# Optimization experiments

Measured on AMD Instinct MI355X. Metric: run time of the kernel, lower is better.

Reference implementation:

```python
import jax, jax.numpy as jnp
import numpy as np

B, S, D, H = 4, 2048, 1024, 16
HD = D // H
SCALE = float(np.sqrt(HD))

def setup_inputs() -> dict:
    key = jax.random.key(0)
    ks = jax.random.split(key, 6)
    std = 1.0 / np.sqrt(D)
    return {
        "x": jax.random.normal(ks[0], (B, S, D), dtype=jnp.float32),
        "Wq": jax.random.normal(ks[1], (D, D), dtype=jnp.float32) * std,
        "Wk": jax.random.normal(ks[2], (D, D), dtype=jnp.float32) * std,
        "Wv": jax.random.normal(ks[3], (D, D), dtype=jnp.float32) * std,
        "Wo": jax.random.normal(ks[4], (D, D), dtype=jnp.float32) * std,
        "bo": jnp.zeros((D,), dtype=jnp.float32),
    }

def reference(x, Wq, Wk, Wv, Wo, bo):
    b, s, _ = x.shape
    # nn.Linear(y) = y @ W.T ; project then split heads -> [B,H,S,HD]
    def proj(W):
        return (x @ W.T).reshape(b, s, H, HD).transpose(0, 2, 1, 3)
    q, k, v = proj(Wq), proj(Wk), proj(Wv)
    scores = jnp.einsum("bhqd,bhkd->bhqk", q, k) / SCALE
    causal = jnp.triu(jnp.ones((s, s), dtype=bool), k=1)
    scores = jnp.where(causal[None, None, :, :], -jnp.inf, scores)
    attn = jax.nn.softmax(scores, axis=-1)  # dropout is identity in eval mode
    out = jnp.einsum("bhqk,bhkd->bhqd", attn, v)
    out = out.transpose(0, 2, 1, 3).reshape(b, s, D)
    return out @ Wo.T + bo
```

## Files before the change

kernel.cpp:

```cpp
#include <hip/hip_runtime.h>
#include <hip/hip_bf16.h>

constexpr int Sc = 2048, Dc = 1024;

typedef __attribute__((ext_vector_type(8))) short bf16x8;
typedef __attribute__((ext_vector_type(4))) short short4v;
typedef __attribute__((ext_vector_type(4))) float f32x4;
typedef __attribute__((ext_vector_type(16))) float f32x16;

static __device__ __forceinline__ short f2bf(float f) {
  __hip_bfloat16 h = __float2bfloat16(f);
  short s; __builtin_memcpy(&s, &h, 2);
  return s;
}

static __device__ __forceinline__ unsigned int cvtpk(float lo, float hi) {
  unsigned int r;
  asm("v_cvt_pk_bf16_f32 %0, %1, %2" : "=v"(r) : "v"(lo), "v"(hi));
  return r;
}

typedef __attribute__((address_space(3))) short lds_short_t;

static __device__ __forceinline__ void gload16(const short* g, lds_short_t* l) {
  __builtin_amdgcn_global_load_lds(
      (const __attribute__((address_space(1))) unsigned int*)g,
      (__attribute__((address_space(3))) unsigned int*)l, 16, 0, 0);
}

__global__ __launch_bounds__(256) void cvt_f32_bf16(const float* __restrict__ src,
                                                    short* __restrict__ dst,
                                                    int n4) {
  int i = blockIdx.x * 256 + threadIdx.x;
  if (i >= n4) return;
  float4 v = ((const float4*)src)[i];
  short4v o;
  o.x = f2bf(v.x); o.y = f2bf(v.y); o.z = f2bf(v.z); o.w = f2bf(v.w);
  ((short4v*)dst)[i] = o;
}

__global__ __launch_bounds__(256) void cvt_w4(const float* __restrict__ w0,
                                              const float* __restrict__ w1,
                                              const float* __restrict__ w2,
                                              const float* __restrict__ w3,
                                              short* __restrict__ dst) {
  const int y = blockIdx.y;
  const float* src = (y == 0) ? w0 : (y == 1) ? w1 : (y == 2) ? w2 : w3;
  int i = blockIdx.x * 256 + threadIdx.x;
  float4 v = ((const float4*)src)[i];
  short4v o;
  o.x = f2bf(v.x); o.y = f2bf(v.y); o.z = f2bf(v.z); o.w = f2bf(v.w);
  ((short4v*)(dst))[(size_t)y * 262144 + i] = o;
}

template <int MODE>
__global__ __launch_bounds__(256) void gemm_mfma(
    const short* __restrict__ A, const short* __restrict__ W,
    const float* __restrict__ bias, short* __restrict__ Qb,
    short* __restrict__ Kb, short* __restrict__ Vt, float* __restrict__ outF) {
  __shared__ short As[128 * 32];
  __shared__ short Bs[128 * 32];
  const int tid = threadIdx.x;
  const int m0 = blockIdx.x * 128, n0 = blockIdx.y * 128;
  const int lane = tid & 63, w = tid >> 6;
  const int wr = w >> 1, wc = w & 1;
  const int ll = lane & 15, lh = lane >> 4;

  lds_short_t* As3 = (lds_short_t*)As;
  lds_short_t* Bs3 = (lds_short_t*)Bs;

  const short* Abase[2];
  const short* Wbase[2];
#pragma unroll
  for (int i = 0; i < 2; ++i) {
    int slot = i * 256 + w * 64 + lane;
    int row = slot >> 2;
    int col = ((slot & 3) ^ (row & 3)) * 8;
    Abase[i] = A + (size_t)(m0 + row) * 1024 + col;
    Wbase[i] = W + (size_t)(n0 + row) * 1024 + col;
  }

  f32x4 acc[4][4] = {};

  for (int k0 = 0; k0 < 1024; k0 += 32) {
    __syncthreads();
#pragma unroll
    for (int i = 0; i < 2; ++i) {
      gload16(Abase[i] + k0, As3 + (i * 256 + w * 64) * 8);
      gload16(Wbase[i] + k0, Bs3 + (i * 256 + w * 64) * 8);
    }
    __syncthreads();

    bf16x8 fa[4], fb[4];
#pragma unroll
    for (int mi = 0; mi < 4; ++mi) {
      int r = wr * 64 + mi * 16 + ll;
      fa[mi] = *(const bf16x8*)&As[r * 32 + ((lh ^ (ll & 3)) * 8)];
    }
#pragma unroll
    for (int ni = 0; ni < 4; ++ni) {
      int r = wc * 64 + ni * 16 + ll;
      fb[ni] = *(const bf16x8*)&Bs[r * 32 + ((lh ^ (ll & 3)) * 8)];
    }
#pragma unroll
    for (int mi = 0; mi < 4; ++mi)
#pragma unroll
      for (int ni = 0; ni < 4; ++ni)
        acc[mi][ni] = __builtin_amdgcn_mfma_f32_16x16x32_bf16(
            fa[mi], fb[ni], acc[mi][ni], 0, 0, 0);
  }

#pragma unroll
  for (int mi = 0; mi < 4; ++mi) {
#pragma unroll
    for (int ni = 0; ni < 4; ++ni) {
#pragma unroll
      for (int r = 0; r < 4; ++r) {
        int row = m0 + wr * 64 + mi * 16 + lh * 4 + r;
        int n = n0 + wc * 64 + ni * 16 + ll;
        float v = acc[mi][ni][r];
        if constexpr (MODE == 1) {
          outF[(size_t)row * 1024 + n] = v + bias[n];
        } else {
          if (n < 1024) {
            Qb[(size_t)row * 1024 + n] = f2bf(v * 0.18033688f);
          } else if (n < 2048) {
            Kb[(size_t)row * 1024 + (n - 1024)] = f2bf(v);
          } else {
            int c = n - 2048, hh = c >> 6, dd = c & 63;
            int bb = row >> 11, ss = row & 2047;
            Vt[(size_t)((bb * 16 + hh) * 64 + dd) * 2048 + ss] = f2bf(v);
          }
        }
      }
    }
  }
}

__global__ __launch_bounds__(256, 3) void attn_v7(const short* __restrict__ Q,
                                                  const short* __restrict__ K,
                                                  const short* __restrict__ Vt,
                                                  short* __restrict__ AO) {
  __shared__ short Ks[2][64 * 64];
  __shared__ short Vs[2][64 * 64];
  const int tid = threadIdx.x, lane = tid & 63, w = tid >> 6;
  const int l31 = lane & 31, lh2 = lane >> 5;
  const int id = blockIdx.x;
  const int bh = id & 63;
  const int qs = id >> 6;
  const int jj = qs >> 2;
  const int qb = (jj == 0) ? qs : (jj == 1) ? 19 - qs : (jj == 2) ? qs - 4 : 23 - qs;
  const int b = bh >> 4, h = bh & 15;
  const int q0 = qb * 128;
  const int R = q0 + w * 32;
  const int kw_last = (R + 31) >> 6;
  const int kb_max = (q0 + 127) >> 6;
  const short* Qp = Q + (size_t)b * Sc * Dc + h * 64;
  const short* Kp = K + (size_t)b * Sc * Dc + h * 64;
  const short* Vp = Vt + (size_t)bh * 64 * Sc;

  lds_short_t* Ks3 = (lds_short_t*)Ks;
  lds_short_t* Vs3 = (lds_short_t*)Vs;

  bf16x8 qf[4];
#pragma unroll
  for (int dk = 0; dk < 4; ++dk)
    qf[dk] = *(const bf16x8*)&Qp[(size_t)(R + l31) * Dc + dk * 16 + lh2 * 8];

  const short* Kst[2];
  const short* Vst[2];
  int ldsOff[2];
#pragma unroll
  for (int i = 0; i < 2; ++i) {
    int slot = i * 256 + w * 64 + lane;
    int row = slot >> 3;
    int col = ((slot & 7) ^ (row & 7)) * 8;
    Kst[i] = Kp + (size_t)row * 1024 + col;
    Vst[i] = Vp + (size_t)row * 2048 + col;
    ldsOff[i] = (i * 256 + w * 64) * 8;
  }

  f32x16 o0 = {}, o1 = {};
  float lrun = 0.f;

#pragma unroll
  for (int i = 0; i < 2; ++i) {
    gload16(Kst[i], Ks3 + ldsOff[i]);
    gload16(Vst[i], Vs3 + ldsOff[i]);
  }
  int cur = 0;

  for (int kb = 0; kb <= kb_max; ++kb) {
    __syncthreads();
    if (kb < kb_max) {
      int nb = cur ^ 1;
#pragma unroll
      for (int i = 0; i < 2; ++i) {
        gload16(Kst[i] + (size_t)(kb + 1) * 65536, Ks3 + nb * 4096 + ldsOff[i]);
        gload16(Vst[i] + (kb + 1) * 64, Vs3 + nb * 4096 + ldsOff[i]);
      }
    }

    if (kb <= kw_last) {
      const bool diag = (kb == kw_last);
      const bool skipHi = diag && ((R & 63) == 0);

      f32x16 sv0 = {}, sv1 = {};
      {
        const int row = l31, rx = row & 7;
#pragma unroll
        for (int dk = 0; dk < 4; ++dk) {
          bf16x8 kf =
              *(const bf16x8*)&Ks[cur][row * 64 + (((dk * 2 + lh2) ^ rx) * 8)];
          sv0 = __builtin_amdgcn_mfma_f32_32x32x16_bf16(kf, qf[dk], sv0, 0, 0, 0);
        }
      }
      if (!skipHi) {
        const int row = 32 + l31, rx = row & 7;
#pragma unroll
        for (int dk = 0; dk < 4; ++dk) {
          bf16x8 kf =
              *(const bf16x8*)&Ks[cur][row * 64 + (((dk * 2 + lh2) ^ rx) * 8)];
          sv1 = __builtin_amdgcn_mfma_f32_32x32x16_bf16(kf, qf[dk], sv1, 0, 0, 0);
        }
      }

      float ts = 0.f;
      if (!diag) {
#pragma unroll
        for (int r = 0; r < 16; ++r) {
          float e0 = exp2f(sv0[r]);
          float e1 = exp2f(sv1[r]);
          sv0[r] = e0; sv1[r] = e1;
          ts += e0 + e1;
        }
      } else if (skipHi) {
#pragma unroll
        for (int r = 0; r < 16; ++r) {
          int kl = (r & 3) + 8 * (r >> 2) + 4 * lh2;
          float e = (kl > l31) ? 0.f : exp2f(sv0[r]);
          sv0[r] = e;
          ts += e;
        }
      } else {
#pragma unroll
        for (int r = 0; r < 16; ++r) {
          float e = exp2f(sv0[r]);
          sv0[r] = e;
          ts += e;
        }
#pragma unroll
        for (int r = 0; r < 16; ++r) {
          int kl = (r & 3) + 8 * (r >> 2) + 4 * lh2;
          float e = (kl > l31) ? 0.f : exp2f(sv1[r]);
          sv1[r] = e;
          ts += e;
        }
      }
      lrun += ts;

      short4v pa[8];
#pragma unroll
      for (int t = 0; t < 4; ++t) {
        union { unsigned int u[2]; short4v s; } pk;
        pk.u[0] = cvtpk(sv0[4 * t + 0], sv0[4 * t + 1]);
        pk.u[1] = cvtpk(sv0[4 * t + 2], sv0[4 * t + 3]);
        pa[t] = pk.s;
      }
      if (skipHi) {
        const int r0 = l31, rx0 = r0 & 7;
        const int r1 = 32 + l31, rx1 = r1 & 7;
#pragma unroll
        for (int t = 0; t < 4; ++t) {
          short4v vb0 =
              *(const short4v*)&Vs[cur][r0 * 64 + ((t ^ rx0) * 8) + lh2 * 4];
          o0 = __builtin_amdgcn_mfma_f32_32x32x8bf16_1k(pa[t], vb0, o0, 0, 0, 0);
          short4v vb1 =
              *(const short4v*)&Vs[cur][r1 * 64 + ((t ^ rx1) * 8) + lh2 * 4];
          o1 = __builtin_amdgcn_mfma_f32_32x32x8bf16_1k(pa[t], vb1, o1, 0, 0, 0);
        }
      } else {
#pragma unroll
        for (int t = 0; t < 4; ++t) {
          union { unsigned int u[2]; short4v s; } pk;
          pk.u[0] = cvtpk(sv1[4 * t + 0], sv1[4 * t + 1]);
          pk.u[1] = cvtpk(sv1[4 * t + 2], sv1[4 * t + 3]);
          pa[4 + t] = pk.s;
        }
        const int r0 = l31, rx0 = r0 & 7;
        const int r1 = 32 + l31, rx1 = r1 & 7;
#pragma unroll
        for (int t = 0; t < 8; ++t) {
          short4v vb0 =
              *(const short4v*)&Vs[cur][r0 * 64 + ((t ^ rx0) * 8) + lh2 * 4];
          o0 = __builtin_amdgcn_mfma_f32_32x32x8bf16_1k(pa[t], vb0, o0, 0, 0, 0);
        }
#pragma unroll
        for (int t = 0; t < 8; ++t) {
          short4v vb1 =
              *(const short4v*)&Vs[cur][r1 * 64 + ((t ^ rx1) * 8) + lh2 * 4];
          o1 = __builtin_amdgcn_mfma_f32_32x32x8bf16_1k(pa[t], vb1, o1, 0, 0, 0);
        }
      }
    }
    cur ^= 1;
  }

  float ltot = lrun + __shfl_xor(lrun, 32);
#pragma unroll
  for (int r = 0; r < 16; ++r) {
    int qr = (r & 3) + 8 * (r >> 2) + 4 * lh2;
    float lq = __shfl(ltot, qr);
    float inv = 1.0f / lq;
    int rowg = R + qr;
    AO[((size_t)(b * Sc + rowg)) * Dc + h * 64 + l31] = f2bf(o0[r] * inv);
    AO[((size_t)(b * Sc + rowg)) * Dc + h * 64 + 32 + l31] = f2bf(o1[r] * inv);
  }
}

extern "C" void kernel_launch(void* const* d_in, const int* in_sizes, int n_in,
                              void* d_out, int out_size, void* d_ws,
                              size_t ws_size, hipStream_t stream) {
  const float* x = (const float*)d_in[0];
  const float* Wq = (const float*)d_in[1];
  const float* Wk = (const float*)d_in[2];
  const float* Wv = (const float*)d_in[3];
  const float* Wo = (const float*)d_in[4];
  const float* bo = (const float*)d_in[5];
  float* out = (float*)d_out;

  short* Qb = (short*)d_out;
  short* Kb = Qb + (size_t)8192 * 1024;
  short* xb = (short*)d_ws;
  short* AOb = xb;
  short* Wc = xb + (size_t)8192 * 1024;
  short* Vt = Wc + (size_t)4096 * 1024;

  dim3 blk(256);
  hipLaunchKernelGGL(cvt_f32_bf16, dim3(8192), blk, 0, stream, x, xb, 2097152);
  hipLaunchKernelGGL(cvt_w4, dim3(1024, 4), blk, 0, stream, Wq, Wk, Wv, Wo, Wc);

  hipLaunchKernelGGL((gemm_mfma<0>), dim3(64, 24), blk, 0, stream, xb, Wc,
                     (const float*)nullptr, Qb, Kb, Vt, (float*)nullptr);

  hipLaunchKernelGGL(attn_v7, dim3(1024), blk, 0, stream, Qb, Kb, Vt, AOb);

  hipLaunchKernelGGL((gemm_mfma<1>), dim3(64, 8), blk, 0, stream, AOb,
                     Wc + (size_t)3072 * 1024, bo, (short*)nullptr,
                     (short*)nullptr, (short*)nullptr, out);
}
```

Measured before the change: 193.3 us.

## Replace QKV projection GEMM with 256x256-tile 8-wave ping-pong kernel

Splits the templated GEMM into a dedicated QKV projection kernel and a separate output-projection kernel. The QKV kernel uses 512 threads and 256x256 output tiles with 64-wide K steps, split into four 128x128 quadrants. Each quadrant's global load into a double-buffered LDS area is interleaved with the MFMA work of another, and s_setprio is raised around the MFMA bursts. It also adds an XCD-aware block remap. The aim is more reuse per loaded tile and better load/compute overlap in the largest GEMM, at the cost of higher register use and 128KB of LDS, which limits occupancy.

```diff
diff --git a/kernel.cpp b/kernel.cpp
--- a/kernel.cpp
+++ b/kernel.cpp
@@ -53,11 +53,197 @@
   ((short4v*)(dst))[(size_t)y * 262144 + i] = o;
 }
 
-template <int MODE>
-__global__ __launch_bounds__(256) void gemm_mfma(
+__global__ __launch_bounds__(512, 2) void gemm_qkv_8p(
     const short* __restrict__ A, const short* __restrict__ W,
-    const float* __restrict__ bias, short* __restrict__ Qb,
-    short* __restrict__ Kb, short* __restrict__ Vt, float* __restrict__ outF) {
+    short* __restrict__ Qb, short* __restrict__ Kb, short* __restrict__ Vt) {
+  __shared__ short lds[2][4][8192];
+  const int tid = threadIdx.x, lane = tid & 63, w = tid >> 6;
+  const int wm = w >> 2, wn = w & 3;
+  const int ll = lane & 15, lh = lane >> 4;
+  const int wg = ((int)blockIdx.x & 7) * 48 + ((int)blockIdx.x >> 3);
+  const int m0 = (wg / 12) * 256, n0 = (wg % 12) * 256;
+
+  lds_short_t* L3 = (lds_short_t*)&lds[0][0][0];
+
+  const short* Asrc[2];
+  const short* Bsrc[2];
+  int dstOff[2];
+#pragma unroll
+  for (int i = 0; i < 2; ++i) {
+    int slot = i * 512 + tid;
+    int ridx = slot >> 3, g = slot & 7;
+    int gp = g ^ (ridx & 7);
+    Asrc[i] = A + (size_t)(m0 + (ridx & 63) + ((ridx >> 6) << 7)) * 1024 + gp * 8;
+    Bsrc[i] = W + (size_t)(n0 + ((ridx >> 5) << 6) + (ridx & 31)) * 1024 + gp * 8;
+    dstOff[i] = (i * 512 + w * 64) * 8;
+  }
+
+  f32x4 acc[8][4] = {};
+  bf16x8 fa[4][2];
+  bf16x8 fb0[2][2];
+  bf16x8 fb1[2][2];
+
+#pragma unroll
+  for (int i = 0; i < 2; ++i) gload16(Asrc[i], L3 + 0 * 8192 + dstOff[i]);
+#pragma unroll
+  for (int i = 0; i < 2; ++i) gload16(Bsrc[i], L3 + 1 * 8192 + dstOff[i]);
+#pragma unroll
+  for (int i = 0; i < 2; ++i)
+    gload16(Bsrc[i] + 32 * 1024, L3 + 2 * 8192 + dstOff[i]);
+#pragma unroll
+  for (int i = 0; i < 2; ++i)
+    gload16(Asrc[i] + 64 * 1024, L3 + 3 * 8192 + dstOff[i]);
+  asm volatile("s_waitcnt vmcnt(4)" ::: "memory");
+  __builtin_amdgcn_s_barrier();
+
+  for (int kt = 0; kt < 16; ++kt) {
+    const int c = kt & 1;
+    const int cb = c * 32768, nb = (c ^ 1) * 32768;
+    const int kn = (kt + 1) * 64;
+
+#pragma unroll
+    for (int mi = 0; mi < 4; ++mi) {
+      int ridx = wm * 64 + mi * 16 + ll;
+#pragma unroll
+      for (int kh = 0; kh < 2; ++kh)
+        fa[mi][kh] = *(const bf16x8*)&lds[c][0][ridx * 64 +
+                                               (((kh * 4 + lh) ^ (ll & 7)) * 8)];
+    }
+#pragma unroll
+    for (int ni = 0; ni < 2; ++ni) {
+      int ridx = wn * 32 + ni * 16 + ll;
+#pragma unroll
+      for (int kh = 0; kh < 2; ++kh)
+        fb0[ni][kh] = *(const bf16x8*)&lds[c][1][ridx * 64 +
+                                                 (((kh * 4 + lh) ^ (ll & 7)) * 8)];
+    }
+    if (kt < 15) {
+#pragma unroll
+      for (int i = 0; i < 2; ++i)
+        gload16(Asrc[i] + kn, L3 + nb + 0 * 8192 + dstOff[i]);
+    }
+    asm volatile("s_waitcnt vmcnt(4)" ::: "memory");
+    __builtin_amdgcn_s_barrier();
+    __builtin_amdgcn_s_setprio(1);
+#pragma unroll
+    for (int mi = 0; mi < 4; ++mi)
+#pragma unroll
+      for (int ni = 0; ni < 2; ++ni)
+#pragma unroll
+        for (int kh = 0; kh < 2; ++kh)
+          acc[mi][ni] = __builtin_amdgcn_mfma_f32_16x16x32_bf16(
+              fa[mi][kh], fb0[ni][kh], acc[mi][ni], 0, 0, 0);
+    __builtin_amdgcn_s_setprio(0);
+    __builtin_amdgcn_s_barrier();
+
+#pragma unroll
+    for (int ni = 0; ni < 2; ++ni) {
+      int ridx = wn * 32 + ni * 16 + ll;
+#pragma unroll
+      for (int kh = 0; kh < 2; ++kh)
+        fb1[ni][kh] = *(const bf16x8*)&lds[c][2][ridx * 64 +
+                                                 (((kh * 4 + lh) ^ (ll & 7)) * 8)];
+    }
+    if (kt < 15) {
+#pragma unroll
+      for (int i = 0; i < 2; ++i)
+        gload16(Bsrc[i] + kn, L3 + nb + 1 * 8192 + dstOff[i]);
+    }
+    asm volatile("s_waitcnt vmcnt(4)" ::: "memory");
+    __builtin_amdgcn_s_barrier();
+    __builtin_amdgcn_s_setprio(1);
+#pragma unroll
+    for (int mi = 0; mi < 4; ++mi)
+#pragma unroll
+      for (int ni = 0; ni < 2; ++ni)
+#pragma unroll
+        for (int kh = 0; kh < 2; ++kh)
+          acc[mi][2 + ni] = __builtin_amdgcn_mfma_f32_16x16x32_bf16(
+              fa[mi][kh], fb1[ni][kh], acc[mi][2 + ni], 0, 0, 0);
+    __builtin_amdgcn_s_setprio(0);
+    __builtin_amdgcn_s_barrier();
+
+#pragma unroll
+    for (int mi = 0; mi < 4; ++mi) {
+      int ridx = wm * 64 + mi * 16 + ll;
+#pragma unroll
+      for (int kh = 0; kh < 2; ++kh)
+        fa[mi][kh] = *(const bf16x8*)&lds[c][3][ridx * 64 +
+                                               (((kh * 4 + lh) ^ (ll & 7)) * 8)];
+    }
+    if (kt < 15) {
+#pragma unroll
+      for (int i = 0; i < 2; ++i)
+        gload16(Bsrc[i] + 32 * 1024 + kn, L3 + nb + 2 * 8192 + dstOff[i]);
+    }
+    asm volatile("s_waitcnt vmcnt(4)" ::: "memory");
+    __builtin_amdgcn_s_barrier();
+    __builtin_amdgcn_s_setprio(1);
+#pragma unroll
+    for (int mi = 0; mi < 4; ++mi)
+#pragma unroll
+      for (int ni = 0; ni < 2; ++ni)
+#pragma unroll
+        for (int kh = 0; kh < 2; ++kh)
+          acc[4 + mi][2 + ni] = __builtin_amdgcn_mfma_f32_16x16x32_bf16(
+              fa[mi][kh], fb1[ni][kh], acc[4 + mi][2 + ni], 0, 0, 0);
+    __builtin_amdgcn_s_setprio(0);
+    __builtin_amdgcn_s_barrier();
+
+#pragma unroll
+    for (int ni = 0; ni < 2; ++ni) {
+      int ridx = wn * 32 + ni * 16 + ll;
+#pragma unroll
+      for (int kh = 0; kh < 2; ++kh)
+        fb0[ni][kh] = *(const bf16x8*)&lds[c][1][ridx * 64 +
+                                                 (((kh * 4 + lh) ^ (ll & 7)) * 8)];
+    }
+    if (kt < 15) {
+#pragma unroll
+      for (int i = 0; i < 2; ++i)
+        gload16(Asrc[i] + 64 * 1024 + kn, L3 + nb + 3 * 8192 + dstOff[i]);
+    }
+    asm volatile("s_waitcnt vmcnt(4)" ::: "memory");
+    __builtin_amdgcn_s_barrier();
+    __builtin_amdgcn_s_setprio(1);
+#pragma unroll
+    for (int mi = 0; mi < 4; ++mi)
+#pragma unroll
+      for (int ni = 0; ni < 2; ++ni)
+#pragma unroll
+        for (int kh = 0; kh < 2; ++kh)
+          acc[4 + mi][ni] = __builtin_amdgcn_mfma_f32_16x16x32_bf16(
+              fa[mi][kh], fb0[ni][kh], acc[4 + mi][ni], 0, 0, 0);
+    __builtin_amdgcn_s_setprio(0);
+    __builtin_amdgcn_s_barrier();
+  }
+
+#pragma unroll
+  for (int mi = 0; mi < 8; ++mi) {
+#pragma unroll
+    for (int ni = 0; ni < 4; ++ni) {
+#pragma unroll
+      for (int r = 0; r < 4; ++r) {
+        int row = m0 + wm * 128 + mi * 16 + lh * 4 + r;
+        int n = n0 + wn * 64 + ni * 16 + ll;
+        float v = acc[mi][ni][r];
+        if (n < 1024) {
+          Qb[(size_t)row * 1024 + n] = f2bf(v * 0.18033688f);
+        } else if (n < 2048) {
+          Kb[(size_t)row * 1024 + (n - 1024)] = f2bf(v);
+        } else {
+          int cc = n - 2048, hh = cc >> 6, dd = cc & 63;
+          int bb = row >> 11, ss = row & 2047;
+          Vt[(size_t)((bb * 16 + hh) * 64 + dd) * 2048 + ss] = f2bf(v);
+        }
+      }
+    }
+  }
+}
+
+__global__ __launch_bounds__(256) void gemm_out(
+    const short* __restrict__ A, const short* __restrict__ W,
+    const float* __restrict__ bias, float* __restrict__ outF) {
   __shared__ short As[128 * 32];
   __shared__ short Bs[128 * 32];
   const int tid = threadIdx.x;
@@ -111,30 +297,15 @@
   }
 
 #pragma unroll
-  for (int mi = 0; mi < 4; ++mi) {
-#pragma unroll
-    for (int ni = 0; ni < 4; ++ni) {
+  for (int mi = 0; mi < 4; ++mi)
+#pragma unroll
+    for (int ni = 0; ni < 4; ++ni)
 #pragma unroll
       for (int r = 0; r < 4; ++r) {
         int row = m0 + wr * 64 + mi * 16 + lh * 4 + r;
         int n = n0 + wc * 64 + ni * 16 + ll;
-        float v = acc[mi][ni][r];
-        if constexpr (MODE == 1) {
-          outF[(size_t)row * 1024 + n] = v + bias[n];
-        } else {
-          if (n < 1024) {
-            Qb[(size_t)row * 1024 + n] = f2bf(v * 0.18033688f);
-          } else if (n < 2048) {
-            Kb[(size_t)row * 1024 + (n - 1024)] = f2bf(v);
-          } else {
-            int c = n - 2048, hh = c >> 6, dd = c & 63;
-            int bb = row >> 11, ss = row & 2047;
-            Vt[(size_t)((bb * 16 + hh) * 64 + dd) * 2048 + ss] = f2bf(v);
-          }
-        }
-      }
-    }
-  }
+        outF[(size_t)row * 1024 + n] = acc[mi][ni][r] + bias[n];
+      }
 }
 
 __global__ __launch_bounds__(256, 3) void attn_v7(const short* __restrict__ Q,
@@ -340,12 +511,11 @@
   hipLaunchKernelGGL(cvt_f32_bf16, dim3(8192), blk, 0, stream, x, xb, 2097152);
   hipLaunchKernelGGL(cvt_w4, dim3(1024, 4), blk, 0, stream, Wq, Wk, Wv, Wo, Wc);
 
-  hipLaunchKernelGGL((gemm_mfma<0>), dim3(64, 24), blk, 0, stream, xb, Wc,
-                     (const float*)nullptr, Qb, Kb, Vt, (float*)nullptr);
+  hipLaunchKernelGGL(gemm_qkv_8p, dim3(384), dim3(512), 0, stream, xb, Wc, Qb,
+                     Kb, Vt);
 
   hipLaunchKernelGGL(attn_v7, dim3(1024), blk, 0, stream, Qb, Kb, Vt, AOb);
 
-  hipLaunchKernelGGL((gemm_mfma<1>), dim3(64, 8), blk, 0, stream, AOb,
-                     Wc + (size_t)3072 * 1024, bo, (short*)nullptr,
-                     (short*)nullptr, (short*)nullptr, out);
-}
+  hipLaunchKernelGGL(gemm_out, dim3(64, 8), blk, 0, stream, AOb,
+                     Wc + (size_t)3072 * 1024, bo, out);
+}
```

After: 201.5 us. +4.2%, slower.
